# Kernel tuning notes

Measured on AMD Instinct MI355X. Metric: run time of the kernel, lower is better.

The kernel has to match this reference:

```python
import jax, jax.numpy as jnp
import numpy as np

N_SENT = 262144
N_BAGS = 4096
HIDDEN = 256
HIER = 2
LAYER0 = 14
NUM_CLASSES = 53


def setup_inputs() -> dict:
    key = jax.random.key(0)
    ks = jax.random.split(key, 8)
    x = jax.random.normal(ks[0], (N_SENT, HIDDEN), dtype=jnp.float32)
    rel_emb0 = jax.random.normal(ks[1], (LAYER0, HIDDEN), dtype=jnp.float32) * 0.1
    rel_emb1 = jax.random.normal(ks[2], (NUM_CLASSES, HIDDEN), dtype=jnp.float32) * 0.1
    disc = jax.random.normal(ks[3], (NUM_CLASSES, 2 * HIDDEN), dtype=jnp.float32) * 0.05
    bias = jnp.zeros((NUM_CLASSES,), dtype=jnp.float32)
    # relation_levels[r] = (coarse node id, fine node id) for relation r
    relation_levels = jnp.stack(
        [jax.random.randint(ks[4], (NUM_CLASSES,), 0, LAYER0, dtype=jnp.int32),
         jnp.arange(NUM_CLASSES, dtype=jnp.int32)], axis=1)
    label_index = jax.random.randint(ks[5], (N_SENT,), 0, NUM_CLASSES, dtype=jnp.int32)
    # ragged bag boundaries: scope[0]=0, scope[-1]=N_SENT, interior sorted
    interior = jnp.sort(jax.random.randint(ks[6], (N_BAGS - 1,), 1, N_SENT, dtype=jnp.int32))
    scope = jnp.concatenate([jnp.zeros((1,), jnp.int32), interior,
                             jnp.full((1,), N_SENT, jnp.int32)])
    return {"x": x, "rel_emb0": rel_emb0, "rel_emb1": rel_emb1, "disc": disc,
            "bias": bias, "relation_levels": relation_levels,
            "label_index": label_index, "scope": scope}


def _segment_ids(scope, n):
    # scope: [B+1] sorted boundaries -> per-sentence bag id [n]
    marks = jnp.zeros((n,), jnp.int32).at[scope[1:-1]].add(1)
    return jnp.cumsum(marks)


def reference(x, rel_emb0, rel_emb1, disc, bias, relation_levels, label_index, scope):
    n = x.shape[0]
    b = scope.shape[0] - 1
    seg = _segment_ids(scope, n)                       # [N]
    ll = relation_levels[label_index]                  # [N, 2]
    # per-level attention logits: <rel_emb[level][node], x>
    lg0 = jnp.sum(rel_emb0[ll[:, 0]] * x, axis=-1)     # [N]
    lg1 = jnp.sum(rel_emb1[ll[:, 1]] * x, axis=-1)     # [N]
    logits = jnp.stack([lg0, lg1], axis=1)             # [N, hier]
    # ragged softmax per bag (stable)
    m = jax.ops.segment_max(logits, seg, num_segments=b)     # [B, hier]
    e = jnp.exp(logits - m[seg])
    s = jax.ops.segment_sum(e, seg, num_segments=b)          # [B, hier]
    score = e / s[seg]                                       # [N, hier]
    # attention-weighted sentence reduction per bag per level
    weighted = score[:, :, None] * x[:, None, :]             # [N, hier, H]
    repre = jax.ops.segment_sum(weighted, seg, num_segments=b)  # [B, hier, H]
    stack_repre = repre.reshape(b, HIER * HIDDEN)            # [B, 2H]
    return stack_repre @ disc.T + bias                       # [B, 53]
```

## Files before the change

### kernel.cpp

```cpp
#include <hip/hip_runtime.h>
#include <math.h>

#define HIDDEN 256
#define NUM_CLASSES 53
#define CHUNK 64
#define CAP 66

__global__ __launch_bounds__(256) void k0_seg(
    const int* __restrict__ scope, int* __restrict__ seg,
    float* __restrict__ s, int n_bags)
{
    const int gtid = blockIdx.x * blockDim.x + threadIdx.x;
    if (gtid < 2 * n_bags) s[gtid] = 0.f;
    const int wid  = gtid >> 6;
    const int lane = gtid & 63;
    if (wid < n_bags) {
        const int st = scope[wid], en = scope[wid + 1];
        for (int i = st + lane; i < en; i += 64) seg[i] = wid;
    }
}

__global__ __launch_bounds__(256) void k1_logits(
    const float* __restrict__ x,
    const float* __restrict__ rel_emb0,
    const float* __restrict__ rel_emb1,
    const int* __restrict__ relation_levels,
    const int* __restrict__ label_index,
    const int* __restrict__ seg,
    float* __restrict__ e,
    float* __restrict__ s)
{
    const int c0   = blockIdx.x * CHUNK;
    const int tid  = threadIdx.x;
    const int lane = tid & 63;
    const int wave = tid >> 6;
    const int half = lane >> 5;
    const int j    = lane & 31;
    const int colb = j * 8;
    const int stream = wave * 2 + half;

    __shared__ float s_local[2 * CAP];
    __shared__ int   s_seg0;
    if (tid == 0) s_seg0 = seg[c0];
    for (int t = tid; t < 2 * CAP; t += 256) s_local[t] = 0.f;
    __syncthreads();
    const int seg0 = s_seg0;

    #pragma unroll
    for (int k = 0; k < CHUNK / 8; ++k) {
        const int row = c0 + 8 * k + stream;
        const float* xp = x + (size_t)row * HIDDEN + colb;
        const float4 xa = *reinterpret_cast<const float4*>(xp);
        const float4 xb = *reinterpret_cast<const float4*>(xp + 4);
        const int lbl = label_index[row];
        const int2 rl = *reinterpret_cast<const int2*>(relation_levels + 2 * lbl);
        const float* p0 = rel_emb0 + (size_t)rl.x * HIDDEN + colb;
        const float* p1 = rel_emb1 + (size_t)rl.y * HIDDEN + colb;
        const float4 r0a = *reinterpret_cast<const float4*>(p0);
        const float4 r0b = *reinterpret_cast<const float4*>(p0 + 4);
        const float4 r1a = *reinterpret_cast<const float4*>(p1);
        const float4 r1b = *reinterpret_cast<const float4*>(p1 + 4);

        float lg0 = xa.x*r0a.x + xa.y*r0a.y + xa.z*r0a.z + xa.w*r0a.w
                  + xb.x*r0b.x + xb.y*r0b.y + xb.z*r0b.z + xb.w*r0b.w;
        float lg1 = xa.x*r1a.x + xa.y*r1a.y + xa.z*r1a.z + xa.w*r1a.w
                  + xb.x*r1b.x + xb.y*r1b.y + xb.z*r1b.z + xb.w*r1b.w;

        #pragma unroll
        for (int off = 16; off > 0; off >>= 1) {
            lg0 += __shfl_xor(lg0, off, 64);
            lg1 += __shfl_xor(lg1, off, 64);
        }

        if (j == 0) {
            const float e0 = __expf(lg0);
            const float e1 = __expf(lg1);
            e[2 * row]     = e0;
            e[2 * row + 1] = e1;
            const int sg = seg[row];
            const int lb = sg - seg0;
            if (lb < CAP) {
                atomicAdd(&s_local[2 * lb],     e0);
                atomicAdd(&s_local[2 * lb + 1], e1);
            } else {
                atomicAdd(&s[2 * sg],     e0);
                atomicAdd(&s[2 * sg + 1], e1);
            }
        }
    }
    __syncthreads();
    for (int t = tid; t < 2 * CAP; t += 256) {
        const float v = s_local[t];
        if (v != 0.f) atomicAdd(&s[2 * seg0 + t], v);
    }
}

__global__ __launch_bounds__(256) void k2_weighted(
    const float* __restrict__ x,
    const float* __restrict__ e,
    const float* __restrict__ s,
    const float* __restrict__ disc,
    const float* __restrict__ bias,
    const int* __restrict__ scope,
    float* __restrict__ out)
{
    const int bag   = blockIdx.x;
    const int start = scope[bag];
    const int end   = scope[bag + 1];

    const int tid  = threadIdx.x;
    const int lane = tid & 63;
    const int wave = tid >> 6;
    const int half = lane >> 5;
    const int j    = lane & 31;
    const int colb = j * 8;
    const int stream = wave * 2 + half;

    const float sv0 = s[2 * bag], sv1 = s[2 * bag + 1];
    const float i0 = (end > start) ? 1.f / sv0 : 0.f;
    const float i1 = (end > start) ? 1.f / sv1 : 0.f;

    float4 a0 = make_float4(0,0,0,0), b0 = make_float4(0,0,0,0);
    float4 a1 = make_float4(0,0,0,0), b1 = make_float4(0,0,0,0);

    for (int r = start + stream; r < end; r += 16) {
        const int r2  = r + 8;
        const bool v2 = (r2 < end);
        const int r2c = v2 ? r2 : r;

        const float2 ew1 = *reinterpret_cast<const float2*>(e + 2 * r);
        const float2 ew2 = *reinterpret_cast<const float2*>(e + 2 * r2c);
        const float* xp1 = x + (size_t)r   * HIDDEN + colb;
        const float* xp2 = x + (size_t)r2c * HIDDEN + colb;
        const float4 x1a = *reinterpret_cast<const float4*>(xp1);
        const float4 x1b = *reinterpret_cast<const float4*>(xp1 + 4);
        const float4 x2a = *reinterpret_cast<const float4*>(xp2);
        const float4 x2b = *reinterpret_cast<const float4*>(xp2 + 4);

        const float w10 = ew1.x * i0, w11 = ew1.y * i1;
        const float w20 = v2 ? ew2.x * i0 : 0.f;
        const float w21 = v2 ? ew2.y * i1 : 0.f;

        a0.x += w10*x1a.x + w20*x2a.x;  a0.y += w10*x1a.y + w20*x2a.y;
        a0.z += w10*x1a.z + w20*x2a.z;  a0.w += w10*x1a.w + w20*x2a.w;
        b0.x += w10*x1b.x + w20*x2b.x;  b0.y += w10*x1b.y + w20*x2b.y;
        b0.z += w10*x1b.z + w20*x2b.z;  b0.w += w10*x1b.w + w20*x2b.w;
        a1.x += w11*x1a.x + w21*x2a.x;  a1.y += w11*x1a.y + w21*x2a.y;
        a1.z += w11*x1a.z + w21*x2a.z;  a1.w += w11*x1a.w + w21*x2a.w;
        b1.x += w11*x1b.x + w21*x2b.x;  b1.y += w11*x1b.y + w21*x2b.y;
        b1.z += w11*x1b.z + w21*x2b.z;  b1.w += w11*x1b.w + w21*x2b.w;
    }

    __shared__ float s_o[2][8][HIDDEN];
    __shared__ float s_repre[2 * HIDDEN];
    {
        float4* d0 = reinterpret_cast<float4*>(&s_o[0][stream][colb]);
        d0[0] = a0; d0[1] = b0;
        float4* d1 = reinterpret_cast<float4*>(&s_o[1][stream][colb]);
        d1[0] = a1; d1[1] = b1;
    }
    __syncthreads();
    {
        const int t = tid;
        #pragma unroll
        for (int h = 0; h < 2; ++h) {
            float acc = 0.f;
            #pragma unroll
            for (int w = 0; w < 8; ++w) acc += s_o[h][w][t];
            s_repre[h * HIDDEN + t] = acc;
        }
    }
    __syncthreads();

    for (int c = wave; c < NUM_CLASSES; c += 4) {
        const float* dr = disc + c * (2 * HIDDEN);
        float p = 0.f;
        #pragma unroll
        for (int k = 0; k < 8; ++k) {
            const int idx = lane + k * 64;
            p += s_repre[idx] * dr[idx];
        }
        #pragma unroll
        for (int off = 32; off > 0; off >>= 1)
            p += __shfl_xor(p, off, 64);
        if (lane == 0)
            out[bag * NUM_CLASSES + c] = p + bias[c];
    }
}

extern "C" void kernel_launch(void* const* d_in, const int* in_sizes, int n_in,
                              void* d_out, int out_size, void* d_ws, size_t ws_size,
                              hipStream_t stream) {
    const float* x               = (const float*)d_in[0];
    const float* rel_emb0        = (const float*)d_in[1];
    const float* rel_emb1        = (const float*)d_in[2];
    const float* disc            = (const float*)d_in[3];
    const float* bias            = (const float*)d_in[4];
    const int*   relation_levels = (const int*)d_in[5];
    const int*   label_index     = (const int*)d_in[6];
    const int*   scope           = (const int*)d_in[7];
    float*       out             = (float*)d_out;

    const int n_bags = in_sizes[7] - 1;
    const int n_rows = in_sizes[6];

    float* s_ws  = (float*)d_ws;
    float* e_ws  = s_ws + 2 * n_bags;
    int*   seg   = (int*)(e_ws + 2 * (size_t)n_rows);

    {
        const int waves  = n_bags;
        const int blocks = (waves * 64 + 255) / 256;
        k0_seg<<<blocks, 256, 0, stream>>>(scope, seg, s_ws, n_bags);
    }
    k1_logits<<<n_rows / CHUNK, 256, 0, stream>>>(
        x, rel_emb0, rel_emb1, relation_levels, label_index, seg, e_ws, s_ws);
    k2_weighted<<<n_bags, 256, 0, stream>>>(
        x, e_ws, s_ws, disc, bias, scope, out);
}
```

Baseline: 446.8 us.

## Fuse weighted reduction into logits kernel to read x once

Merges the logits pass and the attention-weighted bag reduction into one kernel. Each 64-row chunk computes exp logits into shared memory, then reuses the rows to accumulate per-bag unnormalized sums, flushed to global repre and s with atomics at bag boundaries. A small head kernel then normalizes and applies disc with one lane per class. This removes the second full pass over x (256 MB) in exchange for many float atomics on repre. Like the code before, it skips the max subtraction in the softmax.

New measurement: 482.3 us. 8.0% more time.

```diff
diff --git a/kernel.cpp b/kernel.cpp
--- a/kernel.cpp
+++ b/kernel.cpp
@@ -4,30 +4,29 @@
 #define HIDDEN 256
 #define NUM_CLASSES 53
 #define CHUNK 64
-#define CAP 66
 
-__global__ __launch_bounds__(256) void k0_seg(
+
+__global__ __launch_bounds__(256) void k0_init(
     const int* __restrict__ scope, int* __restrict__ seg,
-    float* __restrict__ s, int n_bags)
+    float* __restrict__ repre, float* __restrict__ s)
 {
-    const int gtid = blockIdx.x * blockDim.x + threadIdx.x;
-    if (gtid < 2 * n_bags) s[gtid] = 0.f;
-    const int wid  = gtid >> 6;
-    const int lane = gtid & 63;
-    if (wid < n_bags) {
-        const int st = scope[wid], en = scope[wid + 1];
-        for (int i = st + lane; i < en; i += 64) seg[i] = wid;
-    }
+    const int b = blockIdx.x;
+    const int t = threadIdx.x;
+    repre[(size_t)b * 512 + t]       = 0.f;
+    repre[(size_t)b * 512 + 256 + t] = 0.f;
+    if (t < 2) s[2 * b + t] = 0.f;
+    const int st = scope[b], en = scope[b + 1];
+    for (int i = st + t; i < en; i += 256) seg[i] = b;
 }
 
-__global__ __launch_bounds__(256) void k1_logits(
+__global__ __launch_bounds__(256) void k1_main(
     const float* __restrict__ x,
     const float* __restrict__ rel_emb0,
     const float* __restrict__ rel_emb1,
     const int* __restrict__ relation_levels,
     const int* __restrict__ label_index,
     const int* __restrict__ seg,
-    float* __restrict__ e,
+    float* __restrict__ repre,
     float* __restrict__ s)
 {
     const int c0   = blockIdx.x * CHUNK;
@@ -39,12 +38,10 @@
     const int colb = j * 8;
     const int stream = wave * 2 + half;
 
-    __shared__ float s_local[2 * CAP];
-    __shared__ int   s_seg0;
-    if (tid == 0) s_seg0 = seg[c0];
-    for (int t = tid; t < 2 * CAP; t += 256) s_local[t] = 0.f;
-    __syncthreads();
-    const int seg0 = s_seg0;
+    __shared__ float e_lds[CHUNK][2];
+    __shared__ int   s_seg[CHUNK];
+
+    if (tid < CHUNK) s_seg[tid] = seg[c0 + tid];
 
     #pragma unroll
     for (int k = 0; k < CHUNK / 8; ++k) {
@@ -71,120 +68,72 @@
             lg0 += __shfl_xor(lg0, off, 64);
             lg1 += __shfl_xor(lg1, off, 64);
         }
-
         if (j == 0) {
-            const float e0 = __expf(lg0);
-            const float e1 = __expf(lg1);
-            e[2 * row]     = e0;
-            e[2 * row + 1] = e1;
-            const int sg = seg[row];
-            const int lb = sg - seg0;
-            if (lb < CAP) {
-                atomicAdd(&s_local[2 * lb],     e0);
-                atomicAdd(&s_local[2 * lb + 1], e1);
-            } else {
-                atomicAdd(&s[2 * sg],     e0);
-                atomicAdd(&s[2 * sg + 1], e1);
-            }
-        }
-    }
-    __syncthreads();
-    for (int t = tid; t < 2 * CAP; t += 256) {
-        const float v = s_local[t];
-        if (v != 0.f) atomicAdd(&s[2 * seg0 + t], v);
-    }
-}
-
-__global__ __launch_bounds__(256) void k2_weighted(
-    const float* __restrict__ x,
-    const float* __restrict__ e,
-    const float* __restrict__ s,
-    const float* __restrict__ disc,
-    const float* __restrict__ bias,
-    const int* __restrict__ scope,
-    float* __restrict__ out)
-{
-    const int bag   = blockIdx.x;
-    const int start = scope[bag];
-    const int end   = scope[bag + 1];
-
-    const int tid  = threadIdx.x;
-    const int lane = tid & 63;
-    const int wave = tid >> 6;
-    const int half = lane >> 5;
-    const int j    = lane & 31;
-    const int colb = j * 8;
-    const int stream = wave * 2 + half;
-
-    const float sv0 = s[2 * bag], sv1 = s[2 * bag + 1];
-    const float i0 = (end > start) ? 1.f / sv0 : 0.f;
-    const float i1 = (end > start) ? 1.f / sv1 : 0.f;
-
-    float4 a0 = make_float4(0,0,0,0), b0 = make_float4(0,0,0,0);
-    float4 a1 = make_float4(0,0,0,0), b1 = make_float4(0,0,0,0);
-
-    for (int r = start + stream; r < end; r += 16) {
-        const int r2  = r + 8;
-        const bool v2 = (r2 < end);
-        const int r2c = v2 ? r2 : r;
-
-        const float2 ew1 = *reinterpret_cast<const float2*>(e + 2 * r);
-        const float2 ew2 = *reinterpret_cast<const float2*>(e + 2 * r2c);
-        const float* xp1 = x + (size_t)r   * HIDDEN + colb;
-        const float* xp2 = x + (size_t)r2c * HIDDEN + colb;
-        const float4 x1a = *reinterpret_cast<const float4*>(xp1);
-        const float4 x1b = *reinterpret_cast<const float4*>(xp1 + 4);
-        const float4 x2a = *reinterpret_cast<const float4*>(xp2);
-        const float4 x2b = *reinterpret_cast<const float4*>(xp2 + 4);
-
-        const float w10 = ew1.x * i0, w11 = ew1.y * i1;
-        const float w20 = v2 ? ew2.x * i0 : 0.f;
-        const float w21 = v2 ? ew2.y * i1 : 0.f;
-
-        a0.x += w10*x1a.x + w20*x2a.x;  a0.y += w10*x1a.y + w20*x2a.y;
-        a0.z += w10*x1a.z + w20*x2a.z;  a0.w += w10*x1a.w + w20*x2a.w;
-        b0.x += w10*x1b.x + w20*x2b.x;  b0.y += w10*x1b.y + w20*x2b.y;
-        b0.z += w10*x1b.z + w20*x2b.z;  b0.w += w10*x1b.w + w20*x2b.w;
-        a1.x += w11*x1a.x + w21*x2a.x;  a1.y += w11*x1a.y + w21*x2a.y;
-        a1.z += w11*x1a.z + w21*x2a.z;  a1.w += w11*x1a.w + w21*x2a.w;
-        b1.x += w11*x1b.x + w21*x2b.x;  b1.y += w11*x1b.y + w21*x2b.y;
-        b1.z += w11*x1b.z + w21*x2b.z;  b1.w += w11*x1b.w + w21*x2b.w;
-    }
-
-    __shared__ float s_o[2][8][HIDDEN];
-    __shared__ float s_repre[2 * HIDDEN];
-    {
-        float4* d0 = reinterpret_cast<float4*>(&s_o[0][stream][colb]);
-        d0[0] = a0; d0[1] = b0;
-        float4* d1 = reinterpret_cast<float4*>(&s_o[1][stream][colb]);
-        d1[0] = a1; d1[1] = b1;
-    }
-    __syncthreads();
-    {
-        const int t = tid;
-        #pragma unroll
-        for (int h = 0; h < 2; ++h) {
-            float acc = 0.f;
-            #pragma unroll
-            for (int w = 0; w < 8; ++w) acc += s_o[h][w][t];
-            s_repre[h * HIDDEN + t] = acc;
+            e_lds[8 * k + stream][0] = __expf(lg0);
+            e_lds[8 * k + stream][1] = __expf(lg1);
         }
     }
     __syncthreads();
 
-    for (int c = wave; c < NUM_CLASSES; c += 4) {
-        const float* dr = disc + c * (2 * HIDDEN);
+    float acc0 = 0.f, acc1 = 0.f, se0 = 0.f, se1 = 0.f;
+    int curbag = s_seg[0];
+    for (int r = 0; r < CHUNK; ++r) {
+        const float e0 = e_lds[r][0];
+        const float e1 = e_lds[r][1];
+        const float xv = x[(size_t)(c0 + r) * HIDDEN + tid];
+        acc0 += e0 * xv;
+        acc1 += e1 * xv;
+        se0  += e0;
+        se1  += e1;
+        const bool last = (r == CHUNK - 1);
+        if (last || s_seg[r + 1] != curbag) {
+            atomicAdd(&repre[(size_t)curbag * 512 + tid],       acc0);
+            atomicAdd(&repre[(size_t)curbag * 512 + 256 + tid], acc1);
+            if (tid == 0) atomicAdd(&s[2 * curbag],     se0);
+            if (tid == 1) atomicAdd(&s[2 * curbag + 1], se1);
+            acc0 = acc1 = se0 = se1 = 0.f;
+            if (!last) curbag = s_seg[r + 1];
+        }
+    }
+}
+
+__global__ __launch_bounds__(256) void k2_head(
+    const float* __restrict__ repre,
+    const float* __restrict__ s,
+    const float* __restrict__ disc,
+    const float* __restrict__ bias,
+    float* __restrict__ out)
+{
+    const int tid  = threadIdx.x;
+    const int lane = tid & 63;
+    const int wave = tid >> 6;
+    const int bag  = blockIdx.x * 4 + wave;
+
+    __shared__ float s_rep[4][2 * HIDDEN];
+
+    const float s0 = s[2 * bag], s1 = s[2 * bag + 1];
+    const float inv0 = (s0 > 0.f) ? 1.f / s0 : 0.f;
+    const float inv1 = (s1 > 0.f) ? 1.f / s1 : 0.f;
+    const float inv  = (lane < 32) ? inv0 : inv1;
+
+    const float4* rp = reinterpret_cast<const float4*>(repre + (size_t)bag * 512 + lane * 8);
+    float4 v0 = rp[0], v1 = rp[1];
+    v0.x *= inv; v0.y *= inv; v0.z *= inv; v0.w *= inv;
+    v1.x *= inv; v1.y *= inv; v1.z *= inv; v1.w *= inv;
+    float4* dst = reinterpret_cast<float4*>(&s_rep[wave][lane * 8]);
+    dst[0] = v0; dst[1] = v1;
+
+    if (lane < NUM_CLASSES) {
+        const float4* dr = reinterpret_cast<const float4*>(disc + (size_t)lane * 512);
+        const float4* rr = reinterpret_cast<const float4*>(s_rep[wave]);
         float p = 0.f;
-        #pragma unroll
-        for (int k = 0; k < 8; ++k) {
-            const int idx = lane + k * 64;
-            p += s_repre[idx] * dr[idx];
+        #pragma unroll 8
+        for (int k = 0; k < 128; ++k) {
+            const float4 d = dr[k];
+            const float4 r = rr[k];
+            p += d.x * r.x + d.y * r.y + d.z * r.z + d.w * r.w;
         }
-        #pragma unroll
-        for (int off = 32; off > 0; off >>= 1)
-            p += __shfl_xor(p, off, 64);
-        if (lane == 0)
-            out[bag * NUM_CLASSES + c] = p + bias[c];
+        out[bag * NUM_CLASSES + lane] = p + bias[lane];
     }
 }
 
@@ -204,17 +153,12 @@
     const int n_bags = in_sizes[7] - 1;
     const int n_rows = in_sizes[6];
 
-    float* s_ws  = (float*)d_ws;
-    float* e_ws  = s_ws + 2 * n_bags;
-    int*   seg   = (int*)(e_ws + 2 * (size_t)n_rows);
+    float* repre = (float*)d_ws;
+    float* s_ws  = repre + (size_t)n_bags * 512;
+    int*   seg   = (int*)(s_ws + 2 * n_bags);
 
-    {
-        const int waves  = n_bags;
-        const int blocks = (waves * 64 + 255) / 256;
-        k0_seg<<<blocks, 256, 0, stream>>>(scope, seg, s_ws, n_bags);
-    }
-    k1_logits<<<n_rows / CHUNK, 256, 0, stream>>>(
-        x, rel_emb0, rel_emb1, relation_levels, label_index, seg, e_ws, s_ws);
-    k2_weighted<<<n_bags, 256, 0, stream>>>(
-        x, e_ws, s_ws, disc, bias, scope, out);
+    k0_init<<<n_bags, 256, 0, stream>>>(scope, seg, repre, s_ws);
+    k1_main<<<n_rows / CHUNK, 256, 0, stream>>>(
+        x, rel_emb0, rel_emb1, relation_levels, label_index, seg, repre, s_ws);
+    k2_head<<<n_bags / 4, 256, 0, stream>>>(repre, s_ws, disc, bias, out);
 }
```
